# Kernel optimization log

Hardware: AMD Instinct MI355X
Metric: run time of the kernel (lower is better)

The kernel has to match this reference:

```python
import jax, jax.numpy as jnp
import numpy as np

DIM = 1024
INTER = 2048
N_EXPERTS = 8
TOP_K = 2
ROUTE_SCALE = 1.0


def setup_inputs() -> dict:
    key = jax.random.key(0)
    ks = jax.random.split(key, 4)
    x = jax.random.normal(ks[0], (4, 2048, DIM), dtype=jnp.float32)
    # Gate weight matches nn.Parameter(torch.randn(n_experts, dim))
    Wg = jax.random.normal(ks[1], (N_EXPERTS, DIM), dtype=jnp.float32)
    W1 = jax.random.normal(ks[2], (N_EXPERTS, DIM, INTER), dtype=jnp.float32) * (1.0 / np.sqrt(DIM))
    b1 = jnp.zeros((N_EXPERTS, INTER), dtype=jnp.float32)
    W2 = jax.random.normal(ks[3], (N_EXPERTS, INTER, DIM), dtype=jnp.float32) * (1.0 / np.sqrt(INTER))
    b2 = jnp.zeros((N_EXPERTS, DIM), dtype=jnp.float32)
    return {"x": x, "Wg": Wg, "W1": W1, "b1": b1, "W2": W2, "b2": b2}


def reference(x, Wg, W1, b1, W2, b2):
    # Flatten tokens: [T, D]
    xt = x.reshape(-1, DIM)
    T = xt.shape[0]

    # --- Gate: sigmoid scores, top-k, normalized weights ---
    scores = jax.nn.sigmoid(xt @ Wg.T)                       # [T, E]
    top_w, top_idx = jax.lax.top_k(scores, TOP_K)            # [T, K]
    top_w = top_w / jnp.sum(top_w, axis=-1, keepdims=True)
    top_w = top_w * ROUTE_SCALE

    # Sparse combine weights [T, E] (top_k indices are distinct per token)
    cw = jnp.zeros((T, N_EXPERTS), dtype=xt.dtype)
    cw = cw.at[jnp.arange(T)[:, None], top_idx].set(top_w)

    # --- Experts: dense per-expert MLP, weighted combine ---
    # (dropout is identity in eval mode)
    h = jax.nn.relu(jnp.einsum('td,edh->eth', xt, W1) + b1[:, None, :])   # [E, T, H]
    eo = jnp.einsum('eth,ehd->etd', h, W2) + b2[:, None, :]               # [E, T, D]
    y = jnp.einsum('etd,te->td', eo, cw)                                  # [T, D]
    return y
```

## Files before the change

### kernel.cpp

```cpp
#include <hip/hip_runtime.h>
#include <stdint.h>

#define DIM   1024
#define INTER 2048
#define NEXP  8

typedef _Float16 f16;
typedef __attribute__((ext_vector_type(4))) _Float16 f16x4;
typedef __attribute__((ext_vector_type(8))) _Float16 f16x8;
typedef __attribute__((ext_vector_type(4))) float    f32x4;

static __device__ __forceinline__ void gload16(const void* gsrc, void* lds) {
    __builtin_amdgcn_global_load_lds(
        (const __attribute__((address_space(1))) uint32_t*)gsrc,
        (__attribute__((address_space(3))) uint32_t*)lds,
        16, 0, 0);
}

__global__ void gate_convert_kernel(const float* __restrict__ x, const float* __restrict__ Wg,
                                    f16* __restrict__ xh, float* __restrict__ gw,
                                    int* __restrict__ gidx, int T) {
    const int tok  = (int)((blockIdx.x * (size_t)blockDim.x + threadIdx.x) >> 6);
    const int lane = threadIdx.x & 63;
    if (tok >= T) return;
    const float4* xr  = (const float4*)(x + (size_t)tok * DIM);
    f16*          xhr = xh + (size_t)tok * DIM;
    float s[NEXP];
    #pragma unroll
    for (int e = 0; e < NEXP; ++e) s[e] = 0.f;
    #pragma unroll
    for (int it = 0; it < 4; ++it) {
        int i = it * 64 + lane;
        float4 xv = xr[i];
        f16x4 hv = { (f16)xv.x, (f16)xv.y, (f16)xv.z, (f16)xv.w };
        *(f16x4*)(xhr + i * 4) = hv;
        #pragma unroll
        for (int e = 0; e < NEXP; ++e) {
            float4 wv = ((const float4*)(Wg + e * DIM))[i];
            s[e] += xv.x * wv.x + xv.y * wv.y + xv.z * wv.z + xv.w * wv.w;
        }
    }
    #pragma unroll
    for (int e = 0; e < NEXP; ++e) {
        #pragma unroll
        for (int off = 32; off > 0; off >>= 1) s[e] += __shfl_xor(s[e], off);
    }
    if (lane == 0) {
        float sc[NEXP];
        #pragma unroll
        for (int e = 0; e < NEXP; ++e) sc[e] = 1.f / (1.f + expf(-s[e]));
        int i0 = 0;
        #pragma unroll
        for (int e = 1; e < NEXP; ++e) if (sc[e] > sc[i0]) i0 = e;
        int i1 = -1;
        #pragma unroll
        for (int e = 0; e < NEXP; ++e) if (e != i0 && (i1 < 0 || sc[e] > sc[i1])) i1 = e;
        float w0 = sc[i0], w1 = sc[i1];
        float inv = 1.f / (w0 + w1);
        gw[2 * tok + 0] = w0 * inv;
        gw[2 * tok + 1] = w1 * inv;
        gidx[2 * tok + 0] = i0;
        gidx[2 * tok + 1] = i1;
    }
}

__global__ void transpose_conv_kernel(const float* __restrict__ W, f16* __restrict__ Wt, int K, int N) {
    __shared__ f16 tile[64][65];
    const int e  = blockIdx.z;
    const int kb = blockIdx.y * 64;
    const int nb = blockIdx.x * 64;
    const int tx = threadIdx.x & 63;
    const int ty = threadIdx.x >> 6;
    const float* We  = W  + (size_t)e * K * N;
    f16*         Wte = Wt + (size_t)e * K * N;
    #pragma unroll
    for (int i = 0; i < 16; ++i) {
        int k = ty + i * 4;
        tile[k][tx] = (f16)We[(size_t)(kb + k) * N + nb + tx];
    }
    __syncthreads();
    #pragma unroll
    for (int i = 0; i < 16; ++i) {
        int n = ty + i * 4;
        Wte[(size_t)(nb + n) * K + kb + tx] = tile[tx][n];
    }
}

__global__ __launch_bounds__(1024)
void route_kernel(const int* __restrict__ gidx, int* __restrict__ offsets,
                  int* __restrict__ tor, int* __restrict__ ros, int T) {
    const int tid  = threadIdx.x;
    const int lane = tid & 63;
    const int wv   = tid >> 6;
    const int NE   = 2 * T;
    __shared__ int wc[16][NEXP];
    __shared__ int rb[NEXP];

    int c[NEXP];
    #pragma unroll
    for (int e = 0; e < NEXP; ++e) c[e] = 0;
    for (int i = tid; i < NE; i += 1024) {
        int g = gidx[i];
        #pragma unroll
        for (int e = 0; e < NEXP; ++e) c[e] += (g == e) ? 1 : 0;
    }
    #pragma unroll
    for (int e = 0; e < NEXP; ++e) {
        #pragma unroll
        for (int off = 32; off > 0; off >>= 1) c[e] += __shfl_xor(c[e], off);
    }
    if (lane == 0) {
        #pragma unroll
        for (int e = 0; e < NEXP; ++e) wc[wv][e] = c[e];
    }
    __syncthreads();
    if (tid == 0) {
        int acc = 0;
        for (int e = 0; e < NEXP; ++e) {
            int t = 0;
            for (int w2 = 0; w2 < 16; ++w2) t += wc[w2][e];
            offsets[e] = acc;
            rb[e] = acc;
            acc += t;
        }
        offsets[NEXP] = acc;
    }
    __syncthreads();

    for (int base = 0; base < NE; base += 1024) {
        int i = base + tid;
        int g = gidx[i];
        int myrank = 0;
        #pragma unroll
        for (int e = 0; e < NEXP; ++e) {
            unsigned long long m = __ballot(g == e);
            if (g == e) myrank = __popcll(m & ((1ull << lane) - 1ull));
            if (lane == 0) wc[wv][e] = __popcll(m);
        }
        __syncthreads();
        int pre = 0;
        for (int w2 = 0; w2 < wv; ++w2) pre += wc[w2][g];
        int pos = rb[g] + pre + myrank;
        tor[pos] = i >> 1;
        ros[i]   = pos;
        __syncthreads();
        if (tid < NEXP) {
            int t = 0;
            for (int w2 = 0; w2 < 16; ++w2) t += wc[w2][tid];
            rb[tid] += t;
        }
        __syncthreads();
    }
}

template<int KD, int ND, bool RELU, bool GATHER>
__global__ __launch_bounds__(256)
void moe_gemm_kernel(const f16* __restrict__ Abase, const f16* __restrict__ Bt,
                     const float* __restrict__ bias, const int* __restrict__ offsets,
                     const int* __restrict__ tok, f16* __restrict__ Cout) {
    const int e      = blockIdx.z;
    const int rowBeg = offsets[e];
    const int rowEnd = offsets[e + 1];
    const int row0   = rowBeg + blockIdx.y * 128;
    if (row0 >= rowEnd) return;
    const int n0   = blockIdx.x * 128;
    const int tid  = threadIdx.x;
    const int lane = tid & 63;
    const int wid  = tid >> 6;
    const int wr   = (wid >> 1) * 64;
    const int wc   = (wid & 1) * 64;

    __shared__ __align__(16) f16 As[128 * 32];
    __shared__ __align__(16) f16 Bs[128 * 32];

    const f16* Bte = Bt + (size_t)e * ND * KD;

    int arow[2];
    #pragma unroll
    for (int i = 0; i < 2; ++i) {
        int c  = i * 256 + tid;
        int r  = c >> 2;
        int gr = row0 + r;
        if (gr >= rowEnd) gr = rowEnd - 1;
        arow[i] = GATHER ? tok[gr] : gr;
    }

    f32x4 acc[4][4] = {};

    const int nK = KD / 32;
    for (int kt = 0; kt < nK; ++kt) {
        const int k0 = kt * 32;
        #pragma unroll
        for (int i = 0; i < 2; ++i) {
            int c  = i * 256 + tid;
            int kc = c & 3;
            gload16(Abase + (size_t)arow[i] * KD + k0 + kc * 8, &As[c * 8]);
        }
        #pragma unroll
        for (int i = 0; i < 2; ++i) {
            int c = i * 256 + tid;
            int r = c >> 2, kc = c & 3;
            gload16(Bte + (size_t)(n0 + r) * KD + k0 + kc * 8, &Bs[c * 8]);
        }
        __syncthreads();

        const int koff = (lane >> 4) * 8;
        f16x8 af[4], bfr[4];
        #pragma unroll
        for (int m = 0; m < 4; ++m)
            af[m] = *(const f16x8*)&As[(wr + m * 16 + (lane & 15)) * 32 + koff];
        #pragma unroll
        for (int n = 0; n < 4; ++n)
            bfr[n] = *(const f16x8*)&Bs[(wc + n * 16 + (lane & 15)) * 32 + koff];
        #pragma unroll
        for (int m = 0; m < 4; ++m)
            #pragma unroll
            for (int n = 0; n < 4; ++n)
                acc[m][n] = __builtin_amdgcn_mfma_f32_16x16x32_f16(af[m], bfr[n], acc[m][n], 0, 0, 0);
        __syncthreads();
    }

    const int rowsValid = rowEnd - row0;
    #pragma unroll
    for (int m = 0; m < 4; ++m) {
        #pragma unroll
        for (int n = 0; n < 4; ++n) {
            #pragma unroll
            for (int j = 0; j < 4; ++j) {
                int rl  = wr + m * 16 + ((lane >> 4) << 2) + j;
                int col = n0 + wc + n * 16 + (lane & 15);
                if (rl < rowsValid) {
                    float v = acc[m][n][j] + bias[e * ND + col];
                    if (RELU) v = fmaxf(v, 0.f);
                    Cout[(size_t)(row0 + rl) * ND + col] = (f16)v;
                }
            }
        }
    }
}

__global__ void combine_kernel(const f16* __restrict__ eo, const int* __restrict__ ros,
                               const float* __restrict__ gw, float* __restrict__ y, int T) {
    int gid = blockIdx.x * 256 + threadIdx.x;
    int t   = gid >> 7;
    if (t >= T) return;
    int c0 = (gid & 127) * 8;
    int r0 = ros[2 * t], r1 = ros[2 * t + 1];
    float w0 = gw[2 * t], w1 = gw[2 * t + 1];
    f16x8 v0 = *(const f16x8*)(eo + (size_t)r0 * DIM + c0);
    f16x8 v1 = *(const f16x8*)(eo + (size_t)r1 * DIM + c0);
    f32x4 o0, o1;
    #pragma unroll
    for (int j = 0; j < 4; ++j) o0[j] = w0 * (float)v0[j] + w1 * (float)v1[j];
    #pragma unroll
    for (int j = 0; j < 4; ++j) o1[j] = w0 * (float)v0[4 + j] + w1 * (float)v1[4 + j];
    *(f32x4*)(y + (size_t)t * DIM + c0)     = o0;
    *(f32x4*)(y + (size_t)t * DIM + c0 + 4) = o1;
}

extern "C" void kernel_launch(void* const* d_in, const int* in_sizes, int n_in,
                              void* d_out, int out_size, void* d_ws, size_t ws_size,
                              hipStream_t stream) {
    const float* x  = (const float*)d_in[0];
    const float* Wg = (const float*)d_in[1];
    const float* W1 = (const float*)d_in[2];
    const float* b1 = (const float*)d_in[3];
    const float* W2 = (const float*)d_in[4];
    const float* b2 = (const float*)d_in[5];
    float* y = (float*)d_out;
    const int T = in_sizes[0] / DIM;

    char* ws = (char*)d_ws;
    size_t off = 0;
    auto alloc = [&](size_t bytes) -> char* {
        char* p = ws + off;
        off += (bytes + 255) & ~(size_t)255;
        return p;
    };
    f16* xh   = (f16*)alloc((size_t)T * DIM * 2);
    f16* w1t  = (f16*)alloc((size_t)NEXP * DIM * INTER * 2);
    f16* w2t  = (f16*)alloc((size_t)NEXP * DIM * INTER * 2);
    f16* h    = (f16*)alloc((size_t)2 * T * INTER * 2);
    f16* eo   = (f16*)alloc((size_t)2 * T * DIM * 2);
    float* gw = (float*)alloc((size_t)T * 2 * 4);
    int* gidx = (int*)alloc((size_t)T * 2 * 4);
    int* ros  = (int*)alloc((size_t)T * 2 * 4);
    int* tor  = (int*)alloc((size_t)2 * T * 4);
    int* offsets = (int*)alloc(64 * 4);

    gate_convert_kernel<<<T / 4, 256, 0, stream>>>(x, Wg, xh, gw, gidx, T);
    transpose_conv_kernel<<<dim3(INTER / 64, DIM / 64, NEXP), 256, 0, stream>>>(W1, w1t, DIM, INTER);
    transpose_conv_kernel<<<dim3(DIM / 64, INTER / 64, NEXP), 256, 0, stream>>>(W2, w2t, INTER, DIM);
    route_kernel<<<1, 1024, 0, stream>>>(gidx, offsets, tor, ros, T);
    moe_gemm_kernel<DIM, INTER, true, true>
        <<<dim3(INTER / 128, 64, NEXP), 256, 0, stream>>>(xh, w1t, b1, offsets, tor, h);
    moe_gemm_kernel<INTER, DIM, false, false>
        <<<dim3(DIM / 128, 64, NEXP), 256, 0, stream>>>(h, w2t, b2, offsets, tor, eo);
    combine_kernel<<<(T * DIM / 8 + 255) / 256, 256, 0, stream>>>(eo, ros, gw, y, T);
}
```

Before: 355.4 us.

## Swizzle LDS tiles and remap MoE GEMM blocks across XCDs

Applies an XOR swizzle to the k-chunk positions when staging A and B tiles into LDS, with matching swizzled read offsets, so the 16-byte fragment reads avoid bank conflicts. The grid is also flattened to 1D, and block IDs are remapped so that consecutive blocks landing on the same XCD (round-robin by bid&7) cover contiguous (expert, row-tile, n-tile) ranges. This is meant to improve L2 reuse of weight and activation tiles. The cost is extra integer index arithmetic per block and per load.

```diff
diff --git a/kernel.cpp b/kernel.cpp
--- a/kernel.cpp
+++ b/kernel.cpp
@@ -153,17 +153,25 @@
     }
 }
 
-template<int KD, int ND, bool RELU, bool GATHER>
+template<int KD, int ND, bool RELU, bool GATHER, int RT>
 __global__ __launch_bounds__(256)
 void moe_gemm_kernel(const f16* __restrict__ Abase, const f16* __restrict__ Bt,
                      const float* __restrict__ bias, const int* __restrict__ offsets,
                      const int* __restrict__ tok, f16* __restrict__ Cout) {
-    const int e      = blockIdx.z;
+    constexpr int NT = ND / 128;
+    const int cpx = (NT * RT * NEXP) >> 3;
+    const int bid = blockIdx.x;
+    const int lg  = (bid & 7) * cpx + (bid >> 3);
+    const int nt  = lg % NT;
+    const int tmp = lg / NT;
+    const int rt  = tmp % RT;
+    const int e   = tmp / RT;
+
     const int rowBeg = offsets[e];
     const int rowEnd = offsets[e + 1];
-    const int row0   = rowBeg + blockIdx.y * 128;
+    const int row0   = rowBeg + rt * 128;
     if (row0 >= rowEnd) return;
-    const int n0   = blockIdx.x * 128;
+    const int n0   = nt * 128;
     const int tid  = threadIdx.x;
     const int lane = tid & 63;
     const int wid  = tid >> 6;
@@ -193,25 +201,25 @@
         #pragma unroll
         for (int i = 0; i < 2; ++i) {
             int c  = i * 256 + tid;
-            int kc = c & 3;
+            int kc = (c & 3) ^ ((c >> 3) & 3);
             gload16(Abase + (size_t)arow[i] * KD + k0 + kc * 8, &As[c * 8]);
         }
         #pragma unroll
         for (int i = 0; i < 2; ++i) {
             int c = i * 256 + tid;
-            int r = c >> 2, kc = c & 3;
+            int r = c >> 2, kc = (c & 3) ^ ((c >> 3) & 3);
             gload16(Bte + (size_t)(n0 + r) * KD + k0 + kc * 8, &Bs[c * 8]);
         }
         __syncthreads();
 
-        const int koff = (lane >> 4) * 8;
+        const int sl   = ((lane >> 4) ^ ((lane >> 1) & 3)) * 8;
         f16x8 af[4], bfr[4];
         #pragma unroll
         for (int m = 0; m < 4; ++m)
-            af[m] = *(const f16x8*)&As[(wr + m * 16 + (lane & 15)) * 32 + koff];
+            af[m] = *(const f16x8*)&As[(wr + m * 16 + (lane & 15)) * 32 + sl];
         #pragma unroll
         for (int n = 0; n < 4; ++n)
-            bfr[n] = *(const f16x8*)&Bs[(wc + n * 16 + (lane & 15)) * 32 + koff];
+            bfr[n] = *(const f16x8*)&Bs[(wc + n * 16 + (lane & 15)) * 32 + sl];
         #pragma unroll
         for (int m = 0; m < 4; ++m)
             #pragma unroll
@@ -292,9 +300,9 @@
     transpose_conv_kernel<<<dim3(INTER / 64, DIM / 64, NEXP), 256, 0, stream>>>(W1, w1t, DIM, INTER);
     transpose_conv_kernel<<<dim3(DIM / 64, INTER / 64, NEXP), 256, 0, stream>>>(W2, w2t, INTER, DIM);
     route_kernel<<<1, 1024, 0, stream>>>(gidx, offsets, tor, ros, T);
-    moe_gemm_kernel<DIM, INTER, true, true>
-        <<<dim3(INTER / 128, 64, NEXP), 256, 0, stream>>>(xh, w1t, b1, offsets, tor, h);
-    moe_gemm_kernel<INTER, DIM, false, false>
-        <<<dim3(DIM / 128, 64, NEXP), 256, 0, stream>>>(h, w2t, b2, offsets, tor, eo);
+    moe_gemm_kernel<DIM, INTER, true, true, 64>
+        <<<dim3((INTER / 128) * 64 * NEXP), 256, 0, stream>>>(xh, w1t, b1, offsets, tor, h);
+    moe_gemm_kernel<INTER, DIM, false, false, 64>
+        <<<dim3((DIM / 128) * 64 * NEXP), 256, 0, stream>>>(h, w2t, b2, offsets, tor, eo);
     combine_kernel<<<(T * DIM / 8 + 255) / 256, 256, 0, stream>>>(eo, ros, gw, y, T);
 }
```

Measured after the change: 371.8 us. 4.6% more time.
